# Kernel tuning notes

Measured on AMD Instinct MI355X. Metric: run time of the kernel, lower is better.

The kernel has to match this reference:

```python
import jax, jax.numpy as jnp
import numpy as np

VOCAB = 128
HID = 1024
STD = 0.01


def setup_inputs() -> dict:
    key = jax.random.key(0)
    ks = jax.random.split(key, 9)
    X = jax.random.randint(ks[0], (64, 512), 0, VOCAB, dtype=jnp.int32)
    def w(k, shape):
        return jax.random.normal(k, shape, dtype=jnp.float32) * STD
    return {
        "X": X,
        # reset gate
        "Wr_x": w(ks[1], (VOCAB, HID)), "Wr_h": w(ks[2], (HID, HID)), "b_r": jnp.zeros(HID, jnp.float32),
        # update gate
        "Wz_x": w(ks[3], (VOCAB, HID)), "Wz_h": w(ks[4], (HID, HID)), "b_z": jnp.zeros(HID, jnp.float32),
        # candidate
        "Wh_x": w(ks[5], (VOCAB, HID)), "Wh_h": w(ks[6], (HID, HID)), "b_h": jnp.zeros(HID, jnp.float32),
        # output head
        "W_o": w(ks[7], (HID, VOCAB)), "b_o": jnp.zeros(VOCAB, jnp.float32),
    }


def reference(X, Wr_x, Wr_h, b_r, Wz_x, Wz_h, b_z, Wh_x, Wh_h, b_h, W_o, b_o):
    B, T = X.shape
    # one-hot encode all timesteps: (T, B, V)
    Xoh = jax.nn.one_hot(X.T, VOCAB, dtype=jnp.float32)

    def step(h, x_t):
        # x_t: (B, V), h: (B, H)
        r = jax.nn.sigmoid(x_t @ Wr_x + h @ Wr_h + b_r)
        z = jax.nn.sigmoid(x_t @ Wz_x + h @ Wz_h + b_z)
        h_tilde = jnp.tanh(x_t @ Wh_x + (r * h) @ Wh_h + b_h)
        h_new = z * h + (1.0 - z) * h_tilde
        out = h_new @ W_o + b_o  # (B, V)
        return h_new, out

    h0 = jnp.zeros((B, HID), jnp.float32)
    _, outs = jax.lax.scan(step, h0, Xoh)  # outs: (T, B, V)
    return jnp.transpose(outs, (1, 0, 2))  # (B, T, V)
```

## Files before the change

kernel.cpp:

```cpp
#include <hip/hip_runtime.h>

#define HID   1024
#define TLEN  512
#define VOC   128
#define NR    32
#define NZ    32
#define NO    8
#define NBLK  (NR + NZ + NO)
#define LDSK  1032
#define HBUF  (64 * HID)
#define NHB   4

typedef __bf16 bf16_t;
typedef __attribute__((ext_vector_type(8))) __bf16 bf16x8;
typedef __attribute__((ext_vector_type(4))) float  f32x4;

__device__ __forceinline__ float sigmoid_fast(float x) {
  return 1.0f / (1.0f + __expf(-x));
}
__device__ __forceinline__ float tanh_fast(float x) {
  float e = __expf(-2.0f * x);
  return (1.0f - e) / (1.0f + e);
}

__device__ __forceinline__ void wait32(const unsigned* flags, unsigned tgt) {
  if ((threadIdx.x >> 6) == 0) {
    const int lane = threadIdx.x & 63;
    for (;;) {
      unsigned g = tgt;
      if (lane < 32)
        g = __hip_atomic_load(&flags[lane], __ATOMIC_RELAXED, __HIP_MEMORY_SCOPE_AGENT);
      if (__all(g >= tgt)) break;
      __builtin_amdgcn_s_sleep(1);
    }
    __builtin_amdgcn_fence(__ATOMIC_ACQUIRE, "agent");
  }
  __syncthreads();
}

__device__ __forceinline__ void wait_rf_of(const unsigned* rfl, const unsigned* ofl,
                                           unsigned tgt, unsigned otgt) {
  if ((threadIdx.x >> 6) == 0) {
    const int lane = threadIdx.x & 63;
    for (;;) {
      bool ok = true;
      if (lane < 32)
        ok = __hip_atomic_load(&rfl[lane], __ATOMIC_RELAXED, __HIP_MEMORY_SCOPE_AGENT) >= tgt;
      else if (lane < 40)
        ok = __hip_atomic_load(&ofl[lane - 32], __ATOMIC_RELAXED, __HIP_MEMORY_SCOPE_AGENT) >= otgt;
      if (__all(ok)) break;
      __builtin_amdgcn_s_sleep(1);
    }
    __builtin_amdgcn_fence(__ATOMIC_ACQUIRE, "agent");
  }
  __syncthreads();
}

__device__ __forceinline__ void publish(unsigned* f, unsigned v) {
  __syncthreads();
  if (threadIdx.x == 0)
    __hip_atomic_store(f, v, __ATOMIC_RELEASE, __HIP_MEMORY_SCOPE_AGENT);
}

__global__ void __launch_bounds__(256)
gru_split(const int* __restrict__ X,
          const float* __restrict__ Wr_x, const float* __restrict__ Wr_h, const float* __restrict__ b_r,
          const float* __restrict__ Wz_x, const float* __restrict__ Wz_h, const float* __restrict__ b_z,
          const float* __restrict__ Wh_x, const float* __restrict__ Wh_h, const float* __restrict__ b_h,
          const float* __restrict__ W_o,  const float* __restrict__ b_o,
          float* __restrict__ out,
          bf16_t* __restrict__ h0, bf16_t* __restrict__ rh_bf,
          unsigned* __restrict__ flags)
{
  __shared__ __align__(16) bf16_t Wbuf[2 * 32 * LDSK];

  unsigned* hfl = flags;
  unsigned* rfl = flags + 64;
  unsigned* ofl = flags + 128;

  const int blk  = blockIdx.x;
  const int tid  = threadIdx.x;
  const int lane = tid & 63;
  const int wv   = tid >> 6;
  const int n16  = lane & 15;
  const int q    = lane >> 4;

  const int aoff = (wv * 16 + n16) * HID + q * 8;

  int bi[4];
#pragma unroll
  for (int i = 0; i < 4; ++i) bi[i] = wv * 16 + q * 4 + i;

  if (blk < NR) {
    const int c0 = blk * 32;
    for (int idx = tid; idx < 32 * HID; idx += 256) {
      int n = idx & 31, k = idx >> 5;
      Wbuf[n * LDSK + k] = (bf16_t)Wr_h[k * HID + c0 + n];
    }
    __syncthreads();

    const int j0 = c0 + n16, j1 = j0 + 16;
    const float br0 = b_r[j0], br1 = b_r[j1];
    const bf16_t* w0 = &Wbuf[n16 * LDSK + q * 8];
    const bf16_t* w1 = &Wbuf[(16 + n16) * LDSK + q * 8];

    for (int t = 0; t < TLEN; ++t) {
      wait32(hfl, (unsigned)t);
      const bf16_t* hslot = h0 + (t & (NHB - 1)) * HBUF;
      int xb[4]; float gx0[4], gx1[4];
#pragma unroll
      for (int i = 0; i < 4; ++i) {
        xb[i]  = X[bi[i] * TLEN + t];
        gx0[i] = Wr_x[xb[i] * HID + j0];
        gx1[i] = Wr_x[xb[i] * HID + j1];
      }
      const bf16_t* hrow = hslot + aoff;
      f32x4 a0 = {0.f,0.f,0.f,0.f}, a1 = {0.f,0.f,0.f,0.f};
#pragma unroll 8
      for (int kk = 0; kk < 32; ++kk) {
        bf16x8 a  = *reinterpret_cast<const bf16x8*>(hrow + kk * 32);
        bf16x8 b0 = *reinterpret_cast<const bf16x8*>(w0 + kk * 32);
        bf16x8 b1 = *reinterpret_cast<const bf16x8*>(w1 + kk * 32);
        a0 = __builtin_amdgcn_mfma_f32_16x16x32_bf16(a, b0, a0, 0, 0, 0);
        a1 = __builtin_amdgcn_mfma_f32_16x16x32_bf16(a, b1, a1, 0, 0, 0);
      }
#pragma unroll
      for (int i = 0; i < 4; ++i) {
        int b = bi[i];
        float r0 = sigmoid_fast(a0[i] + br0 + gx0[i]);
        float r1 = sigmoid_fast(a1[i] + br1 + gx1[i]);
        float h0v = (float)hslot[b * HID + j0];
        float h1v = (float)hslot[b * HID + j1];
        rh_bf[b * HID + j0] = (bf16_t)(r0 * h0v);
        rh_bf[b * HID + j1] = (bf16_t)(r1 * h1v);
      }
      publish(&rfl[blk], (unsigned)(t + 1));
    }
  } else if (blk < NR + NZ) {
    const int zb = blk - NR;
    const int c0 = zb * 32;
    for (int idx = tid; idx < 32 * HID; idx += 256) {
      int n = idx & 31, k = idx >> 5;
      Wbuf[n * LDSK + k]             = (bf16_t)Wz_h[k * HID + c0 + n];
      Wbuf[32 * LDSK + n * LDSK + k] = (bf16_t)Wh_h[k * HID + c0 + n];
    }
    __syncthreads();

    const int j0 = c0 + n16, j1 = j0 + 16;
    const float bz0 = b_z[j0], bz1 = b_z[j1];
    const float bh0 = b_h[j0], bh1 = b_h[j1];
    const bf16_t* wz0 = &Wbuf[n16 * LDSK + q * 8];
    const bf16_t* wz1 = &Wbuf[(16 + n16) * LDSK + q * 8];
    const bf16_t* wh0 = &Wbuf[32 * LDSK + n16 * LDSK + q * 8];
    const bf16_t* wh1 = &Wbuf[32 * LDSK + (16 + n16) * LDSK + q * 8];
    const bf16_t* rhrow = rh_bf + aoff;

    f32x4 hm0 = {0.f,0.f,0.f,0.f}, hm1 = {0.f,0.f,0.f,0.f};

    for (int t = 0; t < TLEN; ++t) {
      wait32(hfl, (unsigned)t);
      int xb[4]; float gz0[4], gz1[4], gh0[4], gh1[4];
#pragma unroll
      for (int i = 0; i < 4; ++i) {
        xb[i]  = X[bi[i] * TLEN + t];
        gz0[i] = Wz_x[xb[i] * HID + j0];
        gz1[i] = Wz_x[xb[i] * HID + j1];
        gh0[i] = Wh_x[xb[i] * HID + j0];
        gh1[i] = Wh_x[xb[i] * HID + j1];
      }
      const bf16_t* hrow = h0 + (t & (NHB - 1)) * HBUF + aoff;
      f32x4 az0 = {0.f,0.f,0.f,0.f}, az1 = {0.f,0.f,0.f,0.f};
#pragma unroll 8
      for (int kk = 0; kk < 32; ++kk) {
        bf16x8 a  = *reinterpret_cast<const bf16x8*>(hrow + kk * 32);
        bf16x8 b0 = *reinterpret_cast<const bf16x8*>(wz0 + kk * 32);
        bf16x8 b1 = *reinterpret_cast<const bf16x8*>(wz1 + kk * 32);
        az0 = __builtin_amdgcn_mfma_f32_16x16x32_bf16(a, b0, az0, 0, 0, 0);
        az1 = __builtin_amdgcn_mfma_f32_16x16x32_bf16(a, b1, az1, 0, 0, 0);
      }
      f32x4 z0, z1;
#pragma unroll
      for (int i = 0; i < 4; ++i) {
        z0[i] = sigmoid_fast(az0[i] + bz0 + gz0[i]);
        z1[i] = sigmoid_fast(az1[i] + bz1 + gz1[i]);
      }

      unsigned otgt = (t >= 3) ? (unsigned)(t - 3) : 0u;
      wait_rf_of(rfl, ofl, (unsigned)(t + 1), otgt);
      f32x4 ah0 = {0.f,0.f,0.f,0.f}, ah1 = {0.f,0.f,0.f,0.f};
#pragma unroll 8
      for (int kk = 0; kk < 32; ++kk) {
        bf16x8 a  = *reinterpret_cast<const bf16x8*>(rhrow + kk * 32);
        bf16x8 b0 = *reinterpret_cast<const bf16x8*>(wh0 + kk * 32);
        bf16x8 b1 = *reinterpret_cast<const bf16x8*>(wh1 + kk * 32);
        ah0 = __builtin_amdgcn_mfma_f32_16x16x32_bf16(a, b0, ah0, 0, 0, 0);
        ah1 = __builtin_amdgcn_mfma_f32_16x16x32_bf16(a, b1, ah1, 0, 0, 0);
      }
      bf16_t* hnext = h0 + ((t + 1) & (NHB - 1)) * HBUF;
#pragma unroll
      for (int i = 0; i < 4; ++i) {
        int b = bi[i];
        float ht0 = tanh_fast(ah0[i] + bh0 + gh0[i]);
        float ht1 = tanh_fast(ah1[i] + bh1 + gh1[i]);
        float hn0 = z0[i] * hm0[i] + (1.f - z0[i]) * ht0;
        float hn1 = z1[i] * hm1[i] + (1.f - z1[i]) * ht1;
        hm0[i] = hn0; hm1[i] = hn1;
        hnext[b * HID + j0] = (bf16_t)hn0;
        hnext[b * HID + j1] = (bf16_t)hn1;
      }
      publish(&hfl[zb], (unsigned)(t + 1));
    }
  } else {
    const int ob = blk - NR - NZ;
    const int c0 = ob * 16;
    for (int idx = tid; idx < 16 * HID; idx += 256) {
      int n = idx & 15, k = idx >> 4;
      Wbuf[n * LDSK + k] = (bf16_t)W_o[k * VOC + c0 + n];
    }
    __syncthreads();

    const int v = c0 + n16;
    const float bos = b_o[v];
    const bf16_t* w0 = &Wbuf[n16 * LDSK + q * 8];

    for (int t = 1; t <= TLEN; ++t) {
      wait32(hfl, (unsigned)t);
      const bf16_t* hrow = h0 + (t & (NHB - 1)) * HBUF + aoff;
      f32x4 acc = {0.f,0.f,0.f,0.f};
#pragma unroll 8
      for (int kk = 0; kk < 32; ++kk) {
        bf16x8 a = *reinterpret_cast<const bf16x8*>(hrow + kk * 32);
        bf16x8 b = *reinterpret_cast<const bf16x8*>(w0 + kk * 32);
        acc = __builtin_amdgcn_mfma_f32_16x16x32_bf16(a, b, acc, 0, 0, 0);
      }
#pragma unroll
      for (int i = 0; i < 4; ++i) {
        int b = bi[i];
        out[(b * TLEN + (t - 1)) * VOC + v] = acc[i] + bos;
      }
      publish(&ofl[ob], (unsigned)t);
    }
  }
}

extern "C" void kernel_launch(void* const* d_in, const int* in_sizes, int n_in,
                              void* d_out, int out_size, void* d_ws, size_t ws_size,
                              hipStream_t stream) {
  const int*   X    = (const int*)d_in[0];
  const float* Wr_x = (const float*)d_in[1];
  const float* Wr_h = (const float*)d_in[2];
  const float* b_r  = (const float*)d_in[3];
  const float* Wz_x = (const float*)d_in[4];
  const float* Wz_h = (const float*)d_in[5];
  const float* b_z  = (const float*)d_in[6];
  const float* Wh_x = (const float*)d_in[7];
  const float* Wh_h = (const float*)d_in[8];
  const float* b_h  = (const float*)d_in[9];
  const float* W_o  = (const float*)d_in[10];
  const float* b_o  = (const float*)d_in[11];

  char* ws = (char*)d_ws;
  unsigned* flags = (unsigned*)ws;
  bf16_t*   h0    = (bf16_t*)(ws + 4096);
  bf16_t*   rh_bf = (bf16_t*)(ws + 4096 + NHB * HBUF * sizeof(bf16_t));

  hipMemsetAsync(ws, 0, 4096 + HBUF * sizeof(bf16_t), stream);

  gru_split<<<NBLK, 256, 0, stream>>>(
      X, Wr_x, Wr_h, b_r, Wz_x, Wz_h, b_z, Wh_x, Wh_h, b_h, W_o, b_o,
      (float*)d_out, h0, rh_bf, flags);
}
```

Baseline: 8.678 ms.

## Replace acquire/release fences with relaxed agent-scope atomic data accesses

Drops the acquire fence after the flag spin-waits and turns the release store into a relaxed store. In their place, every cross-block load and store of the hidden state and r*h goes through relaxed agent-scope atomics, which are meant to bypass the non-coherent cache without a full fence. The weight rows are permuted so each lane owns two adjacent columns, letting hidden-state writes be packed as 32-bit pairs. The hidden ring buffer grows from 4 to 8 slots to give the output blocks more slack. With no acquire/release ordering, correctness now depends on the hardware not reordering memory operations, which is a memory-model risk.

```diff
diff --git a/kernel.cpp b/kernel.cpp
--- a/kernel.cpp
+++ b/kernel.cpp
@@ -9,7 +9,7 @@
 #define NBLK  (NR + NZ + NO)
 #define LDSK  1032
 #define HBUF  (64 * HID)
-#define NHB   4
+#define NHB   8
 
 typedef __bf16 bf16_t;
 typedef __attribute__((ext_vector_type(8))) __bf16 bf16x8;
@@ -21,6 +21,27 @@
 __device__ __forceinline__ float tanh_fast(float x) {
   float e = __expf(-2.0f * x);
   return (1.0f - e) / (1.0f + e);
+}
+
+union FragU { unsigned long long u[2]; bf16x8 v; };
+union PairU { bf16_t b[2]; unsigned u; };
+
+__device__ __forceinline__ bf16x8 ld_frag(const bf16_t* p) {
+  FragU x;
+  x.u[0] = __hip_atomic_load((const unsigned long long*)p,       __ATOMIC_RELAXED, __HIP_MEMORY_SCOPE_AGENT);
+  x.u[1] = __hip_atomic_load((const unsigned long long*)(p + 4), __ATOMIC_RELAXED, __HIP_MEMORY_SCOPE_AGENT);
+  return x.v;
+}
+__device__ __forceinline__ void st_pair(bf16_t* p, float f0, float f1) {
+  PairU c;
+  c.b[0] = (bf16_t)f0;
+  c.b[1] = (bf16_t)f1;
+  __hip_atomic_store((unsigned*)p, c.u, __ATOMIC_RELAXED, __HIP_MEMORY_SCOPE_AGENT);
+}
+__device__ __forceinline__ PairU ld_pair(const bf16_t* p) {
+  PairU c;
+  c.u = __hip_atomic_load((const unsigned*)p, __ATOMIC_RELAXED, __HIP_MEMORY_SCOPE_AGENT);
+  return c;
 }
 
 __device__ __forceinline__ void wait32(const unsigned* flags, unsigned tgt) {
@@ -33,7 +54,6 @@
       if (__all(g >= tgt)) break;
       __builtin_amdgcn_s_sleep(1);
     }
-    __builtin_amdgcn_fence(__ATOMIC_ACQUIRE, "agent");
   }
   __syncthreads();
 }
@@ -51,7 +71,6 @@
       if (__all(ok)) break;
       __builtin_amdgcn_s_sleep(1);
     }
-    __builtin_amdgcn_fence(__ATOMIC_ACQUIRE, "agent");
   }
   __syncthreads();
 }
@@ -59,18 +78,18 @@
 __device__ __forceinline__ void publish(unsigned* f, unsigned v) {
   __syncthreads();
   if (threadIdx.x == 0)
-    __hip_atomic_store(f, v, __ATOMIC_RELEASE, __HIP_MEMORY_SCOPE_AGENT);
+    __hip_atomic_store(f, v, __ATOMIC_RELAXED, __HIP_MEMORY_SCOPE_AGENT);
 }
 
 __global__ void __launch_bounds__(256)
-gru_split(const int* __restrict__ X,
-          const float* __restrict__ Wr_x, const float* __restrict__ Wr_h, const float* __restrict__ b_r,
-          const float* __restrict__ Wz_x, const float* __restrict__ Wz_h, const float* __restrict__ b_z,
-          const float* __restrict__ Wh_x, const float* __restrict__ Wh_h, const float* __restrict__ b_h,
-          const float* __restrict__ W_o,  const float* __restrict__ b_o,
-          float* __restrict__ out,
-          bf16_t* __restrict__ h0, bf16_t* __restrict__ rh_bf,
-          unsigned* __restrict__ flags)
+gru_nofence(const int* __restrict__ X,
+            const float* __restrict__ Wr_x, const float* __restrict__ Wr_h, const float* __restrict__ b_r,
+            const float* __restrict__ Wz_x, const float* __restrict__ Wz_h, const float* __restrict__ b_z,
+            const float* __restrict__ Wh_x, const float* __restrict__ Wh_h, const float* __restrict__ b_h,
+            const float* __restrict__ W_o,  const float* __restrict__ b_o,
+            float* __restrict__ out,
+            bf16_t* __restrict__ h0, bf16_t* __restrict__ rh_bf,
+            unsigned* __restrict__ flags)
 {
   __shared__ __align__(16) bf16_t Wbuf[2 * 32 * LDSK];
 
@@ -95,12 +114,12 @@
     const int c0 = blk * 32;
     for (int idx = tid; idx < 32 * HID; idx += 256) {
       int n = idx & 31, k = idx >> 5;
-      Wbuf[n * LDSK + k] = (bf16_t)Wr_h[k * HID + c0 + n];
+      Wbuf[((n & 1) * 16 + (n >> 1)) * LDSK + k] = (bf16_t)Wr_h[k * HID + c0 + n];
     }
     __syncthreads();
 
-    const int j0 = c0 + n16, j1 = j0 + 16;
-    const float br0 = b_r[j0], br1 = b_r[j1];
+    const int j0 = c0 + 2 * n16;
+    const float br0 = b_r[j0], br1 = b_r[j0 + 1];
     const bf16_t* w0 = &Wbuf[n16 * LDSK + q * 8];
     const bf16_t* w1 = &Wbuf[(16 + n16) * LDSK + q * 8];
 
@@ -112,13 +131,13 @@
       for (int i = 0; i < 4; ++i) {
         xb[i]  = X[bi[i] * TLEN + t];
         gx0[i] = Wr_x[xb[i] * HID + j0];
-        gx1[i] = Wr_x[xb[i] * HID + j1];
+        gx1[i] = Wr_x[xb[i] * HID + j0 + 1];
       }
       const bf16_t* hrow = hslot + aoff;
       f32x4 a0 = {0.f,0.f,0.f,0.f}, a1 = {0.f,0.f,0.f,0.f};
 #pragma unroll 8
       for (int kk = 0; kk < 32; ++kk) {
-        bf16x8 a  = *reinterpret_cast<const bf16x8*>(hrow + kk * 32);
+        bf16x8 a  = ld_frag(hrow + kk * 32);
         bf16x8 b0 = *reinterpret_cast<const bf16x8*>(w0 + kk * 32);
         bf16x8 b1 = *reinterpret_cast<const bf16x8*>(w1 + kk * 32);
         a0 = __builtin_amdgcn_mfma_f32_16x16x32_bf16(a, b0, a0, 0, 0, 0);
@@ -129,10 +148,8 @@
         int b = bi[i];
         float r0 = sigmoid_fast(a0[i] + br0 + gx0[i]);
         float r1 = sigmoid_fast(a1[i] + br1 + gx1[i]);
-        float h0v = (float)hslot[b * HID + j0];
-        float h1v = (float)hslot[b * HID + j1];
-        rh_bf[b * HID + j0] = (bf16_t)(r0 * h0v);
-        rh_bf[b * HID + j1] = (bf16_t)(r1 * h1v);
+        PairU hp = ld_pair(hslot + b * HID + j0);
+        st_pair(rh_bf + b * HID + j0, r0 * (float)hp.b[0], r1 * (float)hp.b[1]);
       }
       publish(&rfl[blk], (unsigned)(t + 1));
     }
@@ -141,14 +158,15 @@
     const int c0 = zb * 32;
     for (int idx = tid; idx < 32 * HID; idx += 256) {
       int n = idx & 31, k = idx >> 5;
-      Wbuf[n * LDSK + k]             = (bf16_t)Wz_h[k * HID + c0 + n];
-      Wbuf[32 * LDSK + n * LDSK + k] = (bf16_t)Wh_h[k * HID + c0 + n];
+      int r = (n & 1) * 16 + (n >> 1);
+      Wbuf[r * LDSK + k]             = (bf16_t)Wz_h[k * HID + c0 + n];
+      Wbuf[32 * LDSK + r * LDSK + k] = (bf16_t)Wh_h[k * HID + c0 + n];
     }
     __syncthreads();
 
-    const int j0 = c0 + n16, j1 = j0 + 16;
-    const float bz0 = b_z[j0], bz1 = b_z[j1];
-    const float bh0 = b_h[j0], bh1 = b_h[j1];
+    const int j0 = c0 + 2 * n16;
+    const float bz0 = b_z[j0], bz1 = b_z[j0 + 1];
+    const float bh0 = b_h[j0], bh1 = b_h[j0 + 1];
     const bf16_t* wz0 = &Wbuf[n16 * LDSK + q * 8];
     const bf16_t* wz1 = &Wbuf[(16 + n16) * LDSK + q * 8];
     const bf16_t* wh0 = &Wbuf[32 * LDSK + n16 * LDSK + q * 8];
@@ -164,15 +182,15 @@
       for (int i = 0; i < 4; ++i) {
         xb[i]  = X[bi[i] * TLEN + t];
         gz0[i] = Wz_x[xb[i] * HID + j0];
-        gz1[i] = Wz_x[xb[i] * HID + j1];
+        gz1[i] = Wz_x[xb[i] * HID + j0 + 1];
         gh0[i] = Wh_x[xb[i] * HID + j0];
-        gh1[i] = Wh_x[xb[i] * HID + j1];
+        gh1[i] = Wh_x[xb[i] * HID + j0 + 1];
       }
       const bf16_t* hrow = h0 + (t & (NHB - 1)) * HBUF + aoff;
       f32x4 az0 = {0.f,0.f,0.f,0.f}, az1 = {0.f,0.f,0.f,0.f};
 #pragma unroll 8
       for (int kk = 0; kk < 32; ++kk) {
-        bf16x8 a  = *reinterpret_cast<const bf16x8*>(hrow + kk * 32);
+        bf16x8 a  = ld_frag(hrow + kk * 32);
         bf16x8 b0 = *reinterpret_cast<const bf16x8*>(wz0 + kk * 32);
         bf16x8 b1 = *reinterpret_cast<const bf16x8*>(wz1 + kk * 32);
         az0 = __builtin_amdgcn_mfma_f32_16x16x32_bf16(a, b0, az0, 0, 0, 0);
@@ -185,12 +203,12 @@
         z1[i] = sigmoid_fast(az1[i] + bz1 + gz1[i]);
       }
 
-      unsigned otgt = (t >= 3) ? (unsigned)(t - 3) : 0u;
+      unsigned otgt = (t >= NHB - 1) ? (unsigned)(t - (NHB - 1)) : 0u;
       wait_rf_of(rfl, ofl, (unsigned)(t + 1), otgt);
       f32x4 ah0 = {0.f,0.f,0.f,0.f}, ah1 = {0.f,0.f,0.f,0.f};
 #pragma unroll 8
       for (int kk = 0; kk < 32; ++kk) {
-        bf16x8 a  = *reinterpret_cast<const bf16x8*>(rhrow + kk * 32);
+        bf16x8 a  = ld_frag(rhrow + kk * 32);
         bf16x8 b0 = *reinterpret_cast<const bf16x8*>(wh0 + kk * 32);
         bf16x8 b1 = *reinterpret_cast<const bf16x8*>(wh1 + kk * 32);
         ah0 = __builtin_amdgcn_mfma_f32_16x16x32_bf16(a, b0, ah0, 0, 0, 0);
@@ -205,8 +223,7 @@
         float hn0 = z0[i] * hm0[i] + (1.f - z0[i]) * ht0;
         float hn1 = z1[i] * hm1[i] + (1.f - z1[i]) * ht1;
         hm0[i] = hn0; hm1[i] = hn1;
-        hnext[b * HID + j0] = (bf16_t)hn0;
-        hnext[b * HID + j1] = (bf16_t)hn1;
+        st_pair(hnext + b * HID + j0, hn0, hn1);
       }
       publish(&hfl[zb], (unsigned)(t + 1));
     }
@@ -229,7 +246,7 @@
       f32x4 acc = {0.f,0.f,0.f,0.f};
 #pragma unroll 8
       for (int kk = 0; kk < 32; ++kk) {
-        bf16x8 a = *reinterpret_cast<const bf16x8*>(hrow + kk * 32);
+        bf16x8 a = ld_frag(hrow + kk * 32);
         bf16x8 b = *reinterpret_cast<const bf16x8*>(w0 + kk * 32);
         acc = __builtin_amdgcn_mfma_f32_16x16x32_bf16(a, b, acc, 0, 0, 0);
       }
@@ -266,7 +283,7 @@
 
   hipMemsetAsync(ws, 0, 4096 + HBUF * sizeof(bf16_t), stream);
 
-  gru_split<<<NBLK, 256, 0, stream>>>(
+  gru_nofence<<<NBLK, 256, 0, stream>>>(
       X, Wr_x, Wr_h, b_r, Wz_x, Wz_h, b_z, Wh_x, Wh_h, b_h, W_o, b_o,
       (float*)d_out, h0, rh_bf, flags);
 }
```

Result: slower. 11.12 ms (+28.1%).
